# Kernel tuning notes

Measured on AMD Instinct MI355X. Metric: run time of the kernel, lower is better.

Reference implementation:

```python
import jax, jax.numpy as jnp
import numpy as np

T, B, N_IN, N_OUT = 100, 512, 512, 512
DT = 1e-3
I0 = 1e-3
KAPPA = (0.75 + 0.66) / 2  # (kappa_n + kappa_p)/2
UT = 25.0e-3
TAU_AMPA = 2e-3 * UT / (KAPPA * 20.0 * I0)
TAU_GABA_B = 2e-3 * UT / (KAPPA * 5.0 * I0)
TAU_SOMA = 2e-3 * UT / (KAPPA * 5.0 * I0)
TAU_AHP = 4e-3 * UT / (KAPPA * 2.0 * I0)
ISOMA_DPI_TAU = 5 * I0
SOMA_REFP = 5e-3 / DT  # 5.0
ISOMA_RESET = 1.2 * I0
VR = ISOMA_DPI_TAU + I0
ISOMA_TH = 2000 * I0
ISOMA_PFB_TH = 1000 * I0
ALPHA_SOMA = 4.0
AMPA_GAIN = 4 * 100 * I0
GABA_B_GAIN = 4 * 100 * I0
AHP_GAIN = 4 * 2 * I0
AHP_JUMP = 4 * I0
ISOMA_PFB_NORM = 20 * I0
ISOMA_PFB_GAIN = 100 * I0


def ste_round(x):
    # straight-through round (Round.apply): round fwd, identity bwd
    return x + jax.lax.stop_gradient(jnp.round(x) - x)


@jax.custom_vjp
def spike(x):
    # fast_sigmoid surrogate spike: heaviside fwd, 1/(10|x|+1)^2 surrogate bwd
    return (x > 0).astype(x.dtype)


def _spike_fwd(x):
    return spike(x), x


def _spike_bwd(x, g):
    return (g / (10.0 * jnp.abs(x) + 1.0) ** 2,)


spike.defvjp(_spike_fwd, _spike_bwd)


def _run(input_ampa, input_gaba_b, weight_ampa, weight_gaba_b):
    batch = input_ampa.shape[1]
    sg = jax.lax.stop_gradient
    wa = ste_round(weight_ampa)
    wg = ste_round(weight_gaba_b)
    dtype = input_ampa.dtype
    init = (
        jnp.full((batch, N_OUT), 1.1 * I0, dtype),   # Isoma_mem
        jnp.full((batch, N_OUT), I0, dtype),          # Iampa
        jnp.full((batch, N_OUT), I0, dtype),          # Igaba_b
        jnp.zeros((batch, N_OUT), dtype),             # Isoma_ahp
        jnp.zeros((batch, N_OUT), dtype),             # refractory
    )

    def step(state, inp):
        Isoma_mem, Iampa, Igaba_b, Isoma_ahp, refractory = state
        xa, xg = inp
        Isoma_pfb = sg(ISOMA_PFB_GAIN / (1.0 + jnp.exp(-(Isoma_mem - ISOMA_PFB_TH) / ISOMA_PFB_NORM)))
        Isoma_ahp_d = sg(Isoma_ahp)
        dAHP = (-AHP_GAIN - Isoma_ahp_d) / (TAU_AHP * (1.0 + AHP_GAIN / Isoma_ahp_d))
        Iin = jnp.maximum(Iampa - Igaba_b + I0, I0)
        Isoma_sum = VR + Isoma_ahp_d - Isoma_pfb
        dIsoma_mem = (ALPHA_SOMA * (Iin - Isoma_sum) - Isoma_sum * Isoma_mem / ISOMA_DPI_TAU) / (
            TAU_SOMA * (1.0 + ALPHA_SOMA * ISOMA_DPI_TAU / sg(Isoma_mem)))
        dIampa = (I0 - Iampa) / TAU_AMPA  # uses pre-injection Iampa
        Iampa = Iampa + AMPA_GAIN * (xa @ wa)
        dIgaba_b = (I0 - Igaba_b) / TAU_GABA_B
        Igaba_b = Igaba_b + GABA_B_GAIN * (xg @ wg)
        refractory = refractory - (refractory > 0).astype(dtype)
        Isoma_mem = Isoma_mem + DT * dIsoma_mem * (refractory <= 0).astype(dtype)
        Isoma_ahp = Isoma_ahp_d + DT * dAHP
        Iampa = Iampa + DT * dIampa
        Igaba_b = Igaba_b + DT * dIgaba_b
        S = spike(Isoma_mem - ISOMA_TH)
        refractory = refractory + jnp.floor(S * SOMA_REFP)  # (S*refP).long()
        Isoma_ahp = Isoma_ahp + AHP_JUMP * S
        Isoma_mem = ISOMA_RESET * S + Isoma_mem * (1.0 - S)
        Isoma_mem = jnp.maximum(Isoma_mem, I0)
        return (Isoma_mem, Iampa, Igaba_b, Isoma_ahp, refractory), S

    _, S_seq = jax.lax.scan(step, init, (input_ampa, input_gaba_b))
    return S_seq  # [T, B, N_OUT]


def setup_inputs() -> dict:
    key = jax.random.key(0)
    k1, k2, k3, k4 = jax.random.split(key, 4)
    return {
        "input_ampa": jax.random.uniform(k1, (T, B, N_IN), jnp.float32),
        "input_gaba_b": jax.random.uniform(k2, (T, B, N_IN), jnp.float32),
        "weight_ampa": jax.random.uniform(k3, (N_IN, N_OUT), jnp.float32),
        "weight_gaba_b": jax.random.uniform(k4, (N_IN, N_OUT), jnp.float32),
    }


def reference(input_ampa, input_gaba_b, weight_ampa, weight_gaba_b):
    return _run(input_ampa, input_gaba_b, weight_ampa, weight_gaba_b)
```

## Files before the change

kernel.cpp:

```cpp
#include <hip/hip_runtime.h>
#include <cmath>

namespace {
constexpr int TT = 100;
constexpr int B = 512;
constexpr int NIN = 512;
constexpr int NOUT = 512;
constexpr int NEURONS = B * NOUT;
constexpr int K3B = 3 * NIN;

constexpr double D_I0 = 1e-3;
constexpr double D_KAPPA = (0.75 + 0.66) / 2.0;
constexpr double D_UT = 25.0e-3;
constexpr float F_I0 = (float)D_I0;
constexpr float F_TAU_AMPA = (float)(2e-3 * D_UT / (D_KAPPA * 20.0 * D_I0));
constexpr float F_TAU_GABA = (float)(2e-3 * D_UT / (D_KAPPA * 5.0 * D_I0));
constexpr float F_TAU_SOMA = (float)(2e-3 * D_UT / (D_KAPPA * 5.0 * D_I0));
constexpr float F_TAU_AHP  = (float)(4e-3 * D_UT / (D_KAPPA * 2.0 * D_I0));
constexpr float F_DPI_TAU  = (float)(5.0 * D_I0);
constexpr float F_RESET    = (float)(1.2 * D_I0);
constexpr float F_VR       = (float)(5.0 * D_I0 + D_I0);
constexpr float F_TH       = (float)(2000.0 * D_I0);
constexpr float F_PFB_TH   = (float)(1000.0 * D_I0);
constexpr float F_ALPHA    = 4.0f;
constexpr float F_AMPA_GAIN = (float)(4.0 * 100.0 * D_I0);
constexpr float F_GABA_GAIN = (float)(4.0 * 100.0 * D_I0);
constexpr float F_AHP_GAIN  = (float)(4.0 * 2.0 * D_I0);
constexpr float F_AHP_JUMP  = (float)(4.0 * D_I0);
constexpr float F_PFB_NORM  = (float)(20.0 * D_I0);
constexpr float F_PFB_GAIN  = (float)(100.0 * D_I0);
constexpr float F_ALPHA_DPI = (float)(4.0 * (5.0 * D_I0));
constexpr float F_DT = 1e-3f;
constexpr float F_INIT_MEM = (float)(1.1 * D_I0);
constexpr float F_INV223 = 1.1920928955078125e-7f;
constexpr unsigned BIAS_MUL = (1u << 14) + (1u << 22);
}

typedef __attribute__((ext_vector_type(4))) int i32x4;

__global__ __launch_bounds__(256) void build_wt(
    const float* __restrict__ Wa, const float* __restrict__ Wg,
    unsigned char* __restrict__ WTa, unsigned char* __restrict__ WTg) {
  const int t = blockIdx.x * 256 + threadIdx.x;
  const float* W = (t >> 15) ? Wg : Wa;
  unsigned char* O = (t >> 15) ? WTg : WTa;
  const int r = t & 32767;
  const int n = r >> 6, k8 = r & 63;
  unsigned char b[8];
#pragma unroll
  for (int j = 0; j < 8; ++j)
    b[j] = (unsigned char)(int)rintf(W[(size_t)(k8 * 8 + j) * 512 + n]);
  const size_t addr = (size_t)(n >> 7) * 65536 + (k8 >> 3) * 8192 +
                      ((n >> 4) & 7) * 1024 + (n & 15) * 64 + (k8 & 7) * 8;
  *(unsigned long long*)(O + addr) = *(unsigned long long*)b;
}

__global__ __launch_bounds__(256) void colsum_w(
    const float* __restrict__ Wa, const float* __restrict__ Wg,
    int* __restrict__ colsum) {
  const int t = blockIdx.x * 256 + threadIdx.x;
  const int z = t >> 9, n = t & 511;
  const float* W = z ? Wg : Wa;
  int s = 0;
  for (int k = 0; k < 512; ++k) s += (int)rintf(W[(size_t)k * 512 + n]);
  colsum[t] = s;
}

__global__ __launch_bounds__(256) void split3(
    const float* __restrict__ XA, const float* __restrict__ XG,
    unsigned char* __restrict__ A4a, unsigned char* __restrict__ A4g, int nwork) {
  int t = blockIdx.x * 256 + threadIdx.x;
  const float* X = XA;
  unsigned char* O = A4a;
  if (t >= nwork) { X = XG; O = A4g; t -= nwork; }
  const int i = t >> 6, g8 = t & 63;
  const float4 v0 = *(const float4*)(X + (size_t)i * 512 + g8 * 8);
  const float4 v1 = *(const float4*)(X + (size_t)i * 512 + g8 * 8 + 4);
  const float a[8] = {v0.x, v0.y, v0.z, v0.w, v1.x, v1.y, v1.z, v1.w};
  unsigned int k[8];
#pragma unroll
  for (int e = 0; e < 8; ++e) k[e] = (unsigned int)rintf(a[e] * 8388608.0f);
  const int rt = i >> 7, ir = i & 127;
  unsigned char* base = O + (size_t)rt * 196608 + (g8 >> 3) * 8192 +
                        (ir >> 4) * 1024 + (ir & 15) * 64 + (g8 & 7) * 8;
  unsigned char b[8];
#pragma unroll
  for (int e = 0; e < 8; ++e) b[e] = (unsigned char)(k[e] & 127u);
  *(unsigned long long*)(base) = *(unsigned long long*)b;
#pragma unroll
  for (int e = 0; e < 8; ++e) b[e] = (unsigned char)(((k[e] >> 7) & 255u) - 128u);
  *(unsigned long long*)(base + 65536) = *(unsigned long long*)b;
#pragma unroll
  for (int e = 0; e < 8; ++e) b[e] = (unsigned char)(((k[e] >> 15) & 255u) - 128u);
  *(unsigned long long*)(base + 131072) = *(unsigned long long*)b;
}

__global__ __launch_bounds__(256) void gemm_i8_lds(
    const unsigned char* __restrict__ A4a, const unsigned char* __restrict__ A4g,
    const unsigned char* __restrict__ WTa, const unsigned char* __restrict__ WTg,
    const int* __restrict__ colsum,
    float* __restrict__ INCa, float* __restrict__ INCg, int nwg) {
  __shared__ __align__(16) unsigned char Bl[65536];
  const int bid = blockIdx.x;
  const int L = (bid & 7) * (nwg >> 3) + (bid >> 3);
  const int m = L >> 3, sub = L & 7;
  const int n = sub & 3, z = sub >> 2;
  const unsigned char* A4 = (z ? A4g : A4a) + (size_t)m * 196608;
  const unsigned char* Bg = (z ? WTg : WTa) + (size_t)n * 65536;
  float* C = z ? INCg : INCa;

  const int tid = threadIdx.x;
  const int lane = tid & 63, wave = tid >> 6;
  const int wr = wave >> 1, wc = wave & 1;
  const int fr = lane & 15, fq = lane >> 4;
  const int loff = fr * 64 + fq * 16;

#pragma unroll
  for (int j = 0; j < 16; ++j) {
    const int idx = j * 256 + tid;
    *(uint4*)&Bl[idx * 16] = *(const uint4*)(Bg + (size_t)idx * 16);
  }

  const unsigned char* Ap[4];
#pragma unroll
  for (int fm = 0; fm < 4; ++fm)
    Ap[fm] = A4 + (wr * 4 + fm) * 1024 + loff;
  const unsigned char* Blp = &Bl[(wc * 4) * 1024 + loff];

  i32x4 fa[3][4];
#pragma unroll
  for (int f = 0; f < 4; ++f) {
    fa[0][f] = *(const i32x4*)(Ap[f] + 131072);
    fa[1][f] = *(const i32x4*)(Ap[f] + 131072 + 8192);
  }
  __syncthreads();

  i32x4 acc[4][4] = {};
  i32x4 fb[2][4];
#pragma unroll
  for (int f = 0; f < 4; ++f)
    fb[0][f] = *(const i32x4*)(Blp + f * 1024);

#pragma unroll
  for (int it = 0; it < 24; ++it) {
    if (it < 22) {
      const int it2 = it + 2;
      const int aoff = (2 - (it2 >> 3)) * 65536 + (it2 & 7) * 8192;
#pragma unroll
      for (int f = 0; f < 4; ++f)
        fa[(it + 2) % 3][f] = *(const i32x4*)(Ap[f] + aoff);
    }
    if (it < 23) {
      const int boff = ((it + 1) & 7) * 8192;
#pragma unroll
      for (int f = 0; f < 4; ++f)
        fb[(it + 1) & 1][f] = *(const i32x4*)(Blp + boff + f * 1024);
    }
#pragma unroll
    for (int fm = 0; fm < 4; ++fm)
#pragma unroll
      for (int fn = 0; fn < 4; ++fn)
        acc[fm][fn] = __builtin_amdgcn_mfma_i32_16x16x64_i8(
            fa[it % 3][fm], fb[it & 1][fn], acc[fm][fn], 0, 0, 0);
    if (it == 7) {
#pragma unroll
      for (int fm = 0; fm < 4; ++fm)
#pragma unroll
        for (int fn = 0; fn < 4; ++fn) acc[fm][fn] = acc[fm][fn] << 8;
    }
    if (it == 15) {
#pragma unroll
      for (int fm = 0; fm < 4; ++fm)
#pragma unroll
        for (int fn = 0; fn < 4; ++fn) acc[fm][fn] = acc[fm][fn] << 7;
    }
  }

  const int crow0 = m * 128 + wr * 64;
  const int ccol0 = n * 128 + wc * 64;
  unsigned bias[4];
#pragma unroll
  for (int fn = 0; fn < 4; ++fn)
    bias[fn] = BIAS_MUL * (unsigned)colsum[z * 512 + ccol0 + fn * 16 + fr];
  __syncthreads();
  float* scratch = (float*)Bl + wave * (16 * 68);
  const int erow = lane >> 4;
  const int ecol = (lane & 15) * 4;
#pragma unroll
  for (int fm = 0; fm < 4; ++fm) {
#pragma unroll
    for (int fn = 0; fn < 4; ++fn)
#pragma unroll
      for (int r = 0; r < 4; ++r) {
        const unsigned tot = (unsigned)acc[fm][fn][r] + bias[fn];
        scratch[(fq * 4 + r) * 68 + fn * 16 + fr] = (float)tot * F_INV223;
      }
    float4 rows[4];
#pragma unroll
    for (int j = 0; j < 4; ++j)
      rows[j] = *(const float4*)&scratch[(erow + 4 * j) * 68 + ecol];
#pragma unroll
    for (int j = 0; j < 4; ++j) {
      const int grow = crow0 + fm * 16 + erow + 4 * j;
      *(float4*)&C[(size_t)grow * NOUT + ccol0 + ecol] = rows[j];
    }
  }
}

__global__ __launch_bounds__(256) void neuron_scan(
    const float* __restrict__ inca, const float* __restrict__ incg,
    float* __restrict__ Sout, float* __restrict__ state, int tc, int first) {
  const int idx = blockIdx.x * 256 + threadIdx.x;
  float mem, ampa, gaba, ahp, refr;
  if (first) {
    mem = F_INIT_MEM; ampa = F_I0; gaba = F_I0; ahp = 0.0f; refr = 0.0f;
  } else {
    mem  = state[idx];
    ampa = state[NEURONS + idx];
    gaba = state[2 * NEURONS + idx];
    ahp  = state[3 * NEURONS + idx];
    refr = state[4 * NEURONS + idx];
  }
  for (int t = 0; t < tc; ++t) {
    const float xa = F_AMPA_GAIN * inca[(size_t)t * NEURONS + idx];
    const float xg = F_GABA_GAIN * incg[(size_t)t * NEURONS + idx];
    const float pfb = F_PFB_GAIN / (1.0f + expf(-(mem - F_PFB_TH) / F_PFB_NORM));
    const float dahp = (-F_AHP_GAIN - ahp) / (F_TAU_AHP * (1.0f + F_AHP_GAIN / ahp));
    const float Iin = fmaxf(ampa - gaba + F_I0, F_I0);
    const float Isum = F_VR + ahp - pfb;
    const float dmem = (F_ALPHA * (Iin - Isum) - Isum * mem / F_DPI_TAU)
                     / (F_TAU_SOMA * (1.0f + F_ALPHA_DPI / mem));
    const float dampa = (F_I0 - ampa) / F_TAU_AMPA;
    ampa = ampa + xa;
    const float dgaba = (F_I0 - gaba) / F_TAU_GABA;
    gaba = gaba + xg;
    refr = refr - (refr > 0.0f ? 1.0f : 0.0f);
    mem = mem + F_DT * dmem * (refr <= 0.0f ? 1.0f : 0.0f);
    ahp = ahp + F_DT * dahp;
    ampa = ampa + F_DT * dampa;
    gaba = gaba + F_DT * dgaba;
    const float S = (mem - F_TH) > 0.0f ? 1.0f : 0.0f;
    refr = refr + floorf(S * 5.0f);
    ahp = ahp + F_AHP_JUMP * S;
    mem = F_RESET * S + mem * (1.0f - S);
    mem = fmaxf(mem, F_I0);
    Sout[(size_t)t * NEURONS + idx] = S;
  }
  state[idx] = mem;
  state[NEURONS + idx] = ampa;
  state[2 * NEURONS + idx] = gaba;
  state[3 * NEURONS + idx] = ahp;
  state[4 * NEURONS + idx] = refr;
}

extern "C" void kernel_launch(void* const* d_in, const int* in_sizes, int n_in,
                              void* d_out, int out_size, void* d_ws, size_t ws_size,
                              hipStream_t stream) {
  const float* XA = (const float*)d_in[0];
  const float* XG = (const float*)d_in[1];
  const float* WA = (const float*)d_in[2];
  const float* WG = (const float*)d_in[3];
  float* S = (float*)d_out;

  int tc = 1;
  const int cands[8] = {100, 50, 25, 20, 10, 5, 2, 1};
  for (int i = 0; i < 8; ++i) {
    const size_t need = 5771264ull + (size_t)cands[i] * 3670016ull;
    if (need <= ws_size) { tc = cands[i]; break; }
  }

  unsigned char* WTa = (unsigned char*)d_ws;
  unsigned char* WTg = WTa + (size_t)NOUT * 512;
  int* colsum = (int*)(WTg + (size_t)NOUT * 512);
  unsigned char* A4a = (unsigned char*)(colsum + 1024);
  unsigned char* A4g = A4a + (size_t)tc * B * K3B;
  float* INCa  = (float*)(A4g + (size_t)tc * B * K3B);
  float* INCg  = INCa + (size_t)tc * NEURONS;
  float* state = INCg + (size_t)tc * NEURONS;

  build_wt<<<256, 256, 0, stream>>>(WA, WG, WTa, WTg);
  colsum_w<<<4, 256, 0, stream>>>(WA, WG, colsum);

  const int nwork = tc * B * (NIN / 8);
  const int splitBlocks = 2 * nwork / 256;
  const int nm = tc * B / 128;
  const int nwg = nm * 8;
  const int nch = TT / tc;
  for (int c = 0; c < nch; ++c) {
    const size_t inOff = (size_t)c * tc * B * NIN;
    split3<<<splitBlocks, 256, 0, stream>>>(XA + inOff, XG + inOff, A4a, A4g, nwork);
    gemm_i8_lds<<<nwg, 256, 0, stream>>>(A4a, A4g, WTa, WTg, colsum, INCa, INCg, nwg);
    neuron_scan<<<NEURONS / 256, 256, 0, stream>>>(
        INCa, INCg, S + (size_t)c * tc * NEURONS, state, tc, c == 0 ? 1 : 0);
  }
}
```

Before: 424.7 us.

## Keep GEMM weight fragments in registers instead of LDS staging

The int8 MFMA GEMM stops staging the 64KB weight tile in shared memory. Each wave now loads all of its weight fragments straight from global memory into 32 registers up front, and the kernel uses only a small LDS scratch buffer for the epilogue. Launch bounds ask for two blocks per CU. This removes the LDS fill, the barriers and the per-iteration LDS reads, and the smaller LDS footprint should allow more resident blocks. The cost is many more VGPRs per thread, which could cause spills, and every wave now reads weights from global or L2 redundantly.

After: 437.1 us. 2.9% more time.

```diff
diff --git a/kernel.cpp b/kernel.cpp
--- a/kernel.cpp
+++ b/kernel.cpp
@@ -95,12 +95,12 @@
   *(unsigned long long*)(base + 131072) = *(unsigned long long*)b;
 }
 
-__global__ __launch_bounds__(256) void gemm_i8_lds(
+__global__ __launch_bounds__(256, 2) void gemm_i8_reg2(
     const unsigned char* __restrict__ A4a, const unsigned char* __restrict__ A4g,
     const unsigned char* __restrict__ WTa, const unsigned char* __restrict__ WTg,
     const int* __restrict__ colsum,
     float* __restrict__ INCa, float* __restrict__ INCg, int nwg) {
-  __shared__ __align__(16) unsigned char Bl[65536];
+  __shared__ float scratch_all[4 * 16 * 68];
   const int bid = blockIdx.x;
   const int L = (bid & 7) * (nwg >> 3) + (bid >> 3);
   const int m = L >> 3, sub = L & 7;
@@ -115,32 +115,24 @@
   const int fr = lane & 15, fq = lane >> 4;
   const int loff = fr * 64 + fq * 16;
 
-#pragma unroll
-  for (int j = 0; j < 16; ++j) {
-    const int idx = j * 256 + tid;
-    *(uint4*)&Bl[idx * 16] = *(const uint4*)(Bg + (size_t)idx * 16);
-  }
-
-  const unsigned char* Ap[4];
-#pragma unroll
-  for (int fm = 0; fm < 4; ++fm)
-    Ap[fm] = A4 + (wr * 4 + fm) * 1024 + loff;
-  const unsigned char* Blp = &Bl[(wc * 4) * 1024 + loff];
+  const unsigned char* A4w = A4 + wr * 4096 + loff;
+  const unsigned char* Bgw = Bg + wc * 4096 + loff;
+
+  i32x4 fbr[32];
+#pragma unroll
+  for (int c = 0; c < 8; ++c)
+#pragma unroll
+    for (int f = 0; f < 4; ++f)
+      fbr[c * 4 + f] = *(const i32x4*)(Bgw + c * 8192 + f * 1024);
 
   i32x4 fa[3][4];
 #pragma unroll
   for (int f = 0; f < 4; ++f) {
-    fa[0][f] = *(const i32x4*)(Ap[f] + 131072);
-    fa[1][f] = *(const i32x4*)(Ap[f] + 131072 + 8192);
-  }
-  __syncthreads();
+    fa[0][f] = *(const i32x4*)(A4w + 131072 + f * 1024);
+    fa[1][f] = *(const i32x4*)(A4w + 131072 + 8192 + f * 1024);
+  }
 
   i32x4 acc[4][4] = {};
-  i32x4 fb[2][4];
-#pragma unroll
-  for (int f = 0; f < 4; ++f)
-    fb[0][f] = *(const i32x4*)(Blp + f * 1024);
-
 #pragma unroll
   for (int it = 0; it < 24; ++it) {
     if (it < 22) {
@@ -148,20 +140,14 @@
       const int aoff = (2 - (it2 >> 3)) * 65536 + (it2 & 7) * 8192;
 #pragma unroll
       for (int f = 0; f < 4; ++f)
-        fa[(it + 2) % 3][f] = *(const i32x4*)(Ap[f] + aoff);
-    }
-    if (it < 23) {
-      const int boff = ((it + 1) & 7) * 8192;
-#pragma unroll
-      for (int f = 0; f < 4; ++f)
-        fb[(it + 1) & 1][f] = *(const i32x4*)(Blp + boff + f * 1024);
+        fa[it2 % 3][f] = *(const i32x4*)(A4w + aoff + f * 1024);
     }
 #pragma unroll
     for (int fm = 0; fm < 4; ++fm)
 #pragma unroll
       for (int fn = 0; fn < 4; ++fn)
         acc[fm][fn] = __builtin_amdgcn_mfma_i32_16x16x64_i8(
-            fa[it % 3][fm], fb[it & 1][fn], acc[fm][fn], 0, 0, 0);
+            fa[it % 3][fm], fbr[(it & 7) * 4 + fn], acc[fm][fn], 0, 0, 0);
     if (it == 7) {
 #pragma unroll
       for (int fm = 0; fm < 4; ++fm)
@@ -182,8 +168,7 @@
 #pragma unroll
   for (int fn = 0; fn < 4; ++fn)
     bias[fn] = BIAS_MUL * (unsigned)colsum[z * 512 + ccol0 + fn * 16 + fr];
-  __syncthreads();
-  float* scratch = (float*)Bl + wave * (16 * 68);
+  float* scratch = scratch_all + wave * (16 * 68);
   const int erow = lane >> 4;
   const int ecol = (lane & 15) * 4;
 #pragma unroll
@@ -289,7 +274,7 @@
   for (int c = 0; c < nch; ++c) {
     const size_t inOff = (size_t)c * tc * B * NIN;
     split3<<<splitBlocks, 256, 0, stream>>>(XA + inOff, XG + inOff, A4a, A4g, nwork);
-    gemm_i8_lds<<<nwg, 256, 0, stream>>>(A4a, A4g, WTa, WTg, colsum, INCa, INCg, nwg);
+    gemm_i8_reg2<<<nwg, 256, 0, stream>>>(A4a, A4g, WTa, WTg, colsum, INCa, INCg, nwg);
     neuron_scan<<<NEURONS / 256, 256, 0, stream>>>(
         INCa, INCg, S + (size_t)c * tc * NEURONS, state, tc, c == 0 ? 1 : 0);
   }
```
